# Performance work log

Measured on AMD Instinct MI355X. Metric: run time of the kernel, lower is better.

## Reference

```python
import jax, jax.numpy as jnp
import numpy as np

B, T, C, F = 32, 512, 256, 512


def setup_inputs() -> dict:
    key = jax.random.key(0)
    k1, k2, k3 = jax.random.split(key, 3)
    x = jax.random.normal(k1, (B, T, F), dtype=jnp.float32)
    # glorot-uniform-ish learned params
    context = jax.random.normal(k2, (C, F), dtype=jnp.float32) * (1.0 / np.sqrt(F))
    W = jax.random.normal(k3, (2 * F, 1), dtype=jnp.float32) * (1.0 / np.sqrt(2 * F))
    b = jnp.zeros((1,), dtype=jnp.float32)
    return {"x": x, "context": context, "W": W, "b": b}


def reference(x, context, W, b):
    # Original: concat(tile(x)->[B,T,C,F], tile(context)->[B,T,C,F]) @ W[2F,1] + b.
    # Decompose W = [W_x; W_c] so the [B,T,C,2F] tensor is never materialized.
    f = x.shape[-1]
    s_x = x @ W[:f] + b            # [B, T, 1]
    s_c = context @ W[f:]          # [C, 1]
    scores = s_x[:, :, None, :] + s_c[None, None, :, :]  # [B, T, C, 1]
    # Keras Activation('softmax') acts on the LAST axis (size 1) -> all ones;
    # computed literally for faithfulness.
    att = jax.nn.softmax(scores, axis=-1)[..., 0]        # [B, T, C]
    # multiply by expanded_x and sum over time axis (axis=1)
    out = jnp.einsum('btc,btf->bcf', att, x)             # [B, C, F]
    return out
```

## Files before the change

kernel.cpp:

```cpp
#include <hip/hip_runtime.h>


#define BB 32
#define TT 512
#define CC 256
#define FF 512
#define F4 (FF / 4)

__global__ __launch_bounds__(128) void colsum_partial(const float4* __restrict__ x4,
                                                      float4* __restrict__ part4,
                                                      int tsplit, int trows) {
    const int blk = blockIdx.x;
    const int j   = threadIdx.x;
    const int b   = blk / tsplit;
    const int ts  = blk - b * tsplit;

    const float4* xp = x4 + (size_t)b * TT * F4 + (size_t)ts * trows * F4 + j;

    float4 a0 = make_float4(0.f, 0.f, 0.f, 0.f);
    float4 a1 = make_float4(0.f, 0.f, 0.f, 0.f);
    int t = 0;
    for (; t + 1 < trows; t += 2) {
        float4 v0 = xp[(size_t)t * F4];
        float4 v1 = xp[(size_t)(t + 1) * F4];
        a0.x += v0.x; a0.y += v0.y; a0.z += v0.z; a0.w += v0.w;
        a1.x += v1.x; a1.y += v1.y; a1.z += v1.z; a1.w += v1.w;
    }
    for (; t < trows; ++t) {
        float4 v0 = xp[(size_t)t * F4];
        a0.x += v0.x; a0.y += v0.y; a0.z += v0.z; a0.w += v0.w;
    }
    float4 acc = make_float4(a0.x + a1.x, a0.y + a1.y, a0.z + a1.z, a0.w + a1.w);
    part4[(size_t)blk * F4 + j] = acc;
}

__global__ __launch_bounds__(256) void bcast_out(const float4* __restrict__ part4,
                                                 float4* __restrict__ out4,
                                                 int tsplit) {
    const int CB = 32;
    const int f4 = threadIdx.x & 127;
    const int cg = threadIdx.x >> 7;
    const int b  = blockIdx.x >> 3;
    const int cb = (blockIdx.x & 7) * CB;

    const float4* pp = part4 + (size_t)b * tsplit * F4 + f4;
    float4 acc = make_float4(0.f, 0.f, 0.f, 0.f);
    for (int ts = 0; ts < tsplit; ++ts) {
        float4 v = pp[(size_t)ts * F4];
        acc.x += v.x; acc.y += v.y; acc.z += v.z; acc.w += v.w;
    }

    float4* op = out4 + (size_t)b * CC * F4 + f4;
    for (int c = cb + cg; c < cb + CB; c += 2) {
        op[(size_t)c * F4] = acc;
    }
}

extern "C" void kernel_launch(void* const* d_in, const int* in_sizes, int n_in,
                              void* d_out, int out_size, void* d_ws, size_t ws_size,
                              hipStream_t stream) {
    const float* x = (const float*)d_in[0];
    float* out = (float*)d_out;

    int tsplit = 32;
    if (ws_size < (size_t)BB * tsplit * FF * sizeof(float)) tsplit = 8;
    if (ws_size < (size_t)BB * tsplit * FF * sizeof(float)) tsplit = 2;
    const int trows = TT / tsplit;

    colsum_partial<<<BB * tsplit, 128, 0, stream>>>(
        (const float4*)x, (float4*)d_ws, tsplit, trows);
    bcast_out<<<BB * (CC / 32), 256, 0, stream>>>(
        (const float4*)d_ws, (float4*)out, tsplit);
}
```

Baseline: 96.78 us.

## Fuse column-sum and broadcast into one kernel via last-block atomic counter

Merges the partial column-sum and the broadcast-to-contexts kernels into a single launch. Each block sums 16 time rows using 256 threads split into two row groups, then increments a per-batch atomic counter. The last block for each batch reduces the partials and writes all 256 context rows. This removes one kernel launch and the dependency gap between the two kernels, but adds a memset launch. The full output write for a batch now falls on a single block, which serializes work that was previously spread across 8 blocks.

```diff
diff --git a/kernel.cpp b/kernel.cpp
--- a/kernel.cpp
+++ b/kernel.cpp
@@ -6,53 +6,66 @@
 #define CC 256
 #define FF 512
 #define F4 (FF / 4)
+#define TSPLIT 32
+#define TROWS (TT / TSPLIT)
 
-__global__ __launch_bounds__(128) void colsum_partial(const float4* __restrict__ x4,
-                                                      float4* __restrict__ part4,
-                                                      int tsplit, int trows) {
-    const int blk = blockIdx.x;
-    const int j   = threadIdx.x;
-    const int b   = blk / tsplit;
-    const int ts  = blk - b * tsplit;
-
-    const float4* xp = x4 + (size_t)b * TT * F4 + (size_t)ts * trows * F4 + j;
-
-    float4 a0 = make_float4(0.f, 0.f, 0.f, 0.f);
-    float4 a1 = make_float4(0.f, 0.f, 0.f, 0.f);
-    int t = 0;
-    for (; t + 1 < trows; t += 2) {
-        float4 v0 = xp[(size_t)t * F4];
-        float4 v1 = xp[(size_t)(t + 1) * F4];
-        a0.x += v0.x; a0.y += v0.y; a0.z += v0.z; a0.w += v0.w;
-        a1.x += v1.x; a1.y += v1.y; a1.z += v1.z; a1.w += v1.w;
-    }
-    for (; t < trows; ++t) {
-        float4 v0 = xp[(size_t)t * F4];
-        a0.x += v0.x; a0.y += v0.y; a0.z += v0.z; a0.w += v0.w;
-    }
-    float4 acc = make_float4(a0.x + a1.x, a0.y + a1.y, a0.z + a1.z, a0.w + a1.w);
-    part4[(size_t)blk * F4 + j] = acc;
+__device__ __forceinline__ void acc4(float4& a, const float4& v) {
+    a.x += v.x; a.y += v.y; a.z += v.z; a.w += v.w;
 }
 
-__global__ __launch_bounds__(256) void bcast_out(const float4* __restrict__ part4,
-                                                 float4* __restrict__ out4,
-                                                 int tsplit) {
-    const int CB = 32;
-    const int f4 = threadIdx.x & 127;
-    const int cg = threadIdx.x >> 7;
-    const int b  = blockIdx.x >> 3;
-    const int cb = (blockIdx.x & 7) * CB;
+__global__ __launch_bounds__(256) void fused_colsum_bcast(
+        const float4* __restrict__ x4,
+        float4* __restrict__ part4,
+        unsigned* __restrict__ counters,
+        float4* __restrict__ out4) {
+    __shared__ float4 lds[F4];
+    __shared__ unsigned s_old;
 
-    const float4* pp = part4 + (size_t)b * tsplit * F4 + f4;
-    float4 acc = make_float4(0.f, 0.f, 0.f, 0.f);
-    for (int ts = 0; ts < tsplit; ++ts) {
-        float4 v = pp[(size_t)ts * F4];
-        acc.x += v.x; acc.y += v.y; acc.z += v.z; acc.w += v.w;
+    const int tid = threadIdx.x;
+    const int f4  = tid & 127;
+    const int tg  = tid >> 7;
+    const int blk = blockIdx.x;
+    const int b   = blk >> 5;
+    const int ts  = blk & 31;
+
+    const float4* xp = x4 + ((size_t)b * TT + (size_t)ts * TROWS + tg * 8) * F4 + f4;
+    float4 a = make_float4(0.f, 0.f, 0.f, 0.f);
+#pragma unroll
+    for (int t = 0; t < 8; ++t) {
+        float4 v = xp[(size_t)t * F4];
+        acc4(a, v);
     }
+    if (tg == 1) lds[f4] = a;
+    __syncthreads();
+    if (tg == 0) {
+        acc4(a, lds[f4]);
+        part4[(size_t)blk * F4 + f4] = a;
+    }
+    __threadfence();
+    __syncthreads();
+    if (tid == 0) s_old = atomicAdd(&counters[b], 1u);
+    __syncthreads();
+    if (s_old != TSPLIT - 1) return;
+
+    __threadfence();
+    const float4* pp = part4 + (size_t)b * TSPLIT * F4 + f4;
+    float4 s = make_float4(0.f, 0.f, 0.f, 0.f);
+    for (int k = tg; k < TSPLIT; k += 2) {
+        float4 v = pp[(size_t)k * F4];
+        acc4(s, v);
+    }
+    if (tg == 1) lds[f4] = s;
+    __syncthreads();
+    if (tg == 0) {
+        acc4(s, lds[f4]);
+        lds[f4] = s;
+    }
+    __syncthreads();
+    s = lds[f4];
 
     float4* op = out4 + (size_t)b * CC * F4 + f4;
-    for (int c = cb + cg; c < cb + CB; c += 2) {
-        op[(size_t)c * F4] = acc;
+    for (int c = tg; c < CC; c += 2) {
+        op[(size_t)c * F4] = s;
     }
 }
 
@@ -62,13 +75,10 @@
     const float* x = (const float*)d_in[0];
     float* out = (float*)d_out;
 
-    int tsplit = 32;
-    if (ws_size < (size_t)BB * tsplit * FF * sizeof(float)) tsplit = 8;
-    if (ws_size < (size_t)BB * tsplit * FF * sizeof(float)) tsplit = 2;
-    const int trows = TT / tsplit;
+    unsigned* counters = (unsigned*)d_ws;
+    float4*   part4    = (float4*)((char*)d_ws + 256);
 
-    colsum_partial<<<BB * tsplit, 128, 0, stream>>>(
-        (const float4*)x, (float4*)d_ws, tsplit, trows);
-    bcast_out<<<BB * (CC / 32), 256, 0, stream>>>(
-        (const float4*)d_ws, (float4*)out, tsplit);
+    hipMemsetAsync(counters, 0, BB * sizeof(unsigned), stream);
+    fused_colsum_bcast<<<BB * TSPLIT, 256, 0, stream>>>(
+        (const float4*)x, part4, counters, (float4*)out);
 }
```

Result: slower. 203.8 us (+110.6%).
